# Kernel tuning notes

Measured on AMD Instinct MI355X. Metric: run time of the kernel, lower is better.

Reference implementation:

```python
import jax, jax.numpy as jnp
import numpy as np

K_NEIGHBORS = 10
SINKHORN_REG = 0.1
SINKHORN_ITERS = 50
EPS = 1e-10


def _pairwise_dist(x):
    # Euclidean cdist; clamp avoids sqrt(0) NaN grads on the diagonal
    sq = jnp.sum(x * x, axis=1)
    d2 = sq[:, None] + sq[None, :] - 2.0 * (x @ x.T)
    return jnp.sqrt(jnp.maximum(d2, 1e-12))


def setup_inputs() -> dict:
    key = jax.random.key(0)
    k1, k2 = jax.random.split(key)
    n, d = 8192, 128
    return {
        "embeddings": jax.random.normal(k1, (n, d), dtype=jnp.float32),
        "reference_embeddings": jax.random.normal(k2, (n, d), dtype=jnp.float32),
    }


def reference(embeddings, reference_embeddings):
    k = min(K_NEIGHBORS, embeddings.shape[0] - 1)

    cur_d = _pairwise_dist(embeddings)              # [n, n]
    ref_d = _pairwise_dist(reference_embeddings)    # [n, n]

    # k+1 smallest (ascending), drop self-distance column
    cur_knn = jnp.sort(cur_d, axis=1)[:, 1:k + 1]   # [n, k]
    ref_knn = jnp.sort(ref_d, axis=1)[:, 1:k + 1]   # [n, k]

    a = cur_knn / (jnp.sum(cur_knn, axis=1, keepdims=True) + EPS)  # [n, k]
    b = ref_knn / (jnp.sum(ref_knn, axis=1, keepdims=True) + EPS)  # [n, k]

    idx = jnp.arange(k, dtype=jnp.float32)
    M = jnp.abs(idx[None, :] - idx[:, None]) / k    # [k, k] shared cost
    Kmat = jnp.exp(-M / SINKHORN_REG)               # [k, k]

    # Batched Sinkhorn across all n samples at once
    def step(u, _):
        v = b / (u @ Kmat + EPS)          # K.T @ u per sample (K symmetric; explicit form u @ K)
        u = a / (v @ Kmat.T + EPS)        # K @ v per sample
        return u, None

    u0 = jnp.ones_like(a)
    u, _ = jax.lax.scan(step, u0, None, length=SINKHORN_ITERS)
    v = b / (u @ Kmat + EPS)

    # sum_ij u_i K_ij M_ij v_j per sample, then mean over n
    per_sample = jnp.einsum('ni,ij,nj->n', u, Kmat * M, v)
    return jnp.mean(per_sample)
```

## Files before the change

kernel.cpp:

```cpp
#include <hip/hip_runtime.h>
#include <hip/hip_bf16.h>
#include <math.h>

#define N 8192
#define D 128
#define NELEM (N * D)
#define KNN 10
#define EPSF 1e-10f
#define RT 64
#define NSLICE 8
#define RH 1024
#define BIGF 3.0e38f

typedef unsigned short ushort_t;
typedef short bf16x8 __attribute__((ext_vector_type(8)));
typedef float f32x4 __attribute__((ext_vector_type(4)));

template <int L>
__device__ __forceinline__ void insM(float (&l)[L], float v) {
  #pragma unroll
  for (int q = L - 1; q >= 1; --q)
    l[q] = __builtin_amdgcn_fmed3f(l[q - 1], l[q], v);
  l[0] = fminf(l[0], v);
}

__global__ void prep_kernel(const float* __restrict__ xc,
                            const float* __restrict__ xr,
                            ushort_t* __restrict__ xb,
                            ushort_t* __restrict__ xa,
                            float* __restrict__ sq) {
  int wid  = (blockIdx.x * blockDim.x + threadIdx.x) >> 6;
  int lane = threadIdx.x & 63;
  if (wid >= 2 * N) return;
  const float* x = (wid < N) ? xc : xr;
  int row = (wid < N) ? wid : wid - N;
  float2 v = *reinterpret_cast<const float2*>(x + (size_t)row * D + lane * 2);
  float s = v.x * v.x + v.y * v.y;
  #pragma unroll
  for (int off = 32; off; off >>= 1) s += __shfl_xor(s, off, 64);
  if (lane == 0) sq[wid] = s;
  auto cvt = [](float f) -> unsigned int {
    unsigned int b = __float_as_uint(f);
    return (b + 0x7FFFu + ((b >> 16) & 1u)) >> 16;
  };
  unsigned int pb = cvt(v.x) | (cvt(v.y) << 16);
  unsigned int pa = cvt(-2.f * v.x) | (cvt(-2.f * v.y) << 16);
  *reinterpret_cast<unsigned int*>(xb + (size_t)wid * D + lane * 2) = pb;
  *reinterpret_cast<unsigned int*>(xa + (size_t)wid * D + lane * 2) = pa;
}

__global__ __launch_bounds__(256, 4) void knn_mfma(
    const ushort_t* __restrict__ xb,
    const ushort_t* __restrict__ xa,
    const float* __restrict__ sq,
    float* __restrict__ partial) {
  __shared__ __align__(16) ushort_t Albuf[2][RT * D];
  __shared__ float sqbuf[2][RT];

  const int bid = blockIdx.x;
  const int mat = bid >> 9;
  const int colblk = (bid >> 3) & 63;
  const int slice = bid & 7;
  const ushort_t* __restrict__ XB = xb + (size_t)mat * NELEM;
  const ushort_t* __restrict__ XA = xa + (size_t)mat * NELEM;
  const float* __restrict__ SQ = sq + mat * N;
  const int r0 = slice * RH;
  const int t = threadIdx.x;
  const int w = t >> 6, l = t & 63;
  const int c0w = colblk * 128 + w * 32;

  bf16x8 bfr[2][4];
  #pragma unroll
  for (int j = 0; j < 2; ++j) {
    const ushort_t* p = XB + (size_t)(c0w + j * 16 + (l & 15)) * D + (l >> 4) * 8;
    #pragma unroll
    for (int kk = 0; kk < 4; ++kk)
      bfr[j][kk] = *reinterpret_cast<const bf16x8*>(p + kk * 32);
  }

  float cand[2][KNN];
  #pragma unroll
  for (int j = 0; j < 2; ++j)
    #pragma unroll
    for (int q = 0; q < KNN; ++q) cand[j][q] = BIGF;

  auto stage = [&](int tt, int bb) {
    const ushort_t* rowg = XA + (size_t)(r0 + tt * RT) * D;
    #pragma unroll
    for (int k2 = 0; k2 < 4; ++k2) {
      int s = w * 256 + k2 * 64 + l;
      int row = s >> 4, chslot = s & 15;
      int ch = (chslot & 8) | ((chslot & 7) ^ (row & 7));
      const ushort_t* g = rowg + row * D + ch * 8;
      ushort_t* dst = &Albuf[bb][(w * 256 + k2 * 64) * 8];
      __builtin_amdgcn_global_load_lds(
          (const __attribute__((address_space(1))) void*)g,
          (__attribute__((address_space(3))) void*)dst, 16, 0, 0);
    }
    if (w == 0) {
      const float* gs = SQ + r0 + tt * RT + l;
      float* dsts = &sqbuf[bb][0];
      __builtin_amdgcn_global_load_lds(
          (const __attribute__((address_space(1))) void*)gs,
          (__attribute__((address_space(3))) void*)dsts, 4, 0, 0);
    }
  };

  stage(0, 0);
  asm volatile("s_waitcnt vmcnt(0)" ::: "memory");
  __syncthreads();

  for (int tt = 0; tt < RH / RT; ++tt) {
    const int cur = tt & 1;
    if (tt < RH / RT - 1) stage(tt + 1, cur ^ 1);

    f32x4 sqi[4];
    #pragma unroll
    for (int i = 0; i < 4; ++i)
      sqi[i] = *reinterpret_cast<const f32x4*>(&sqbuf[cur][i * 16 + (l >> 4) * 4]);

    f32x4 acc[4][2];
    #pragma unroll
    for (int i = 0; i < 4; ++i)
      #pragma unroll
      for (int j = 0; j < 2; ++j) acc[i][j] = sqi[i];

    #pragma unroll
    for (int kk = 0; kk < 4; ++kk) {
      const int ch = kk * 4 + (l >> 4);
      const int chs = (ch & 8) | ((ch & 7) ^ (l & 7));
      bf16x8 af[4];
      #pragma unroll
      for (int i = 0; i < 4; ++i) {
        const int row = i * 16 + (l & 15);
        af[i] = *reinterpret_cast<const bf16x8*>(&Albuf[cur][(row * 16 + chs) * 8]);
      }
      #pragma unroll
      for (int i = 0; i < 4; ++i)
        #pragma unroll
        for (int j = 0; j < 2; ++j)
          acc[i][j] = __builtin_amdgcn_mfma_f32_16x16x32_bf16(af[i], bfr[j][kk],
                                                              acc[i][j], 0, 0, 0);
    }

    const int rbase = r0 + tt * RT;
    const unsigned diff = (unsigned)(c0w - rbase);
    if (diff < 64u) {
      #pragma unroll
      for (int i = 0; i < 4; ++i)
        #pragma unroll
        for (int j = 0; j < 2; ++j) {
          const int rr = (int)diff + j * 16 + (l & 15) - i * 16 - ((l >> 4) << 2);
          #pragma unroll
          for (int r = 0; r < 4; ++r)
            if (rr == r) acc[i][j][r] = BIGF;
        }
    }

    #pragma unroll
    for (int r = 0; r < 4; ++r)
      #pragma unroll
      for (int i = 0; i < 4; ++i)
        #pragma unroll
        for (int j = 0; j < 2; ++j)
          insM<KNN>(cand[j], acc[i][j][r]);

    asm volatile("s_waitcnt vmcnt(0)" ::: "memory");
    __syncthreads();
  }

  #pragma unroll
  for (int step = 16; step <= 32; step <<= 1)
    #pragma unroll
    for (int j = 0; j < 2; ++j)
      #pragma unroll
      for (int q = 0; q < KNN; ++q) {
        float o = __shfl_xor(cand[j][q], step, 64);
        insM<KNN>(cand[j], o);
      }

  if (l < 16) {
    #pragma unroll
    for (int j = 0; j < 2; ++j) {
      const int c = c0w + j * 16 + l;
      float* dst = partial + ((size_t)(mat * N + c) * NSLICE + slice) * KNN;
      #pragma unroll
      for (int q = 0; q < KNN; ++q) dst[q] = cand[j][q];
    }
  }
}

__global__ void merge_kernel(const float* __restrict__ partial,
                             const float* __restrict__ sq,
                             float* __restrict__ knn) {
  int idx = blockIdx.x * blockDim.x + threadIdx.x;
  if (idx >= 2 * N) return;
  float best[KNN];
  #pragma unroll
  for (int q = 0; q < KNN; ++q) best[q] = BIGF;
  const float* p = partial + (size_t)idx * NSLICE * KNN;
  for (int s = 0; s < NSLICE * KNN; ++s) insM<KNN>(best, p[s]);
  const float sqc = sq[idx];
  #pragma unroll
  for (int q = 0; q < KNN; ++q) {
    float d2 = best[q] + sqc;
    knn[(size_t)idx * KNN + q] = sqrtf(fmaxf(d2, 1e-12f));
  }
}

__global__ void sinkhorn_kernel(const float* __restrict__ knnc,
                                const float* __restrict__ knnr,
                                float* __restrict__ ps) {
  int s = blockIdx.x * blockDim.x + threadIdx.x;
  if (s >= N) return;
  constexpr float E1 = 0.36787944117144233f;
  float a[KNN], b[KNN];
  float suma = 0.f, sumb = 0.f;
  #pragma unroll
  for (int q = 0; q < KNN; ++q) { a[q] = knnc[(size_t)s * KNN + q]; suma += a[q]; }
  #pragma unroll
  for (int q = 0; q < KNN; ++q) { b[q] = knnr[(size_t)s * KNN + q]; sumb += b[q]; }
  float rsa = __builtin_amdgcn_rcpf(suma + EPSF);
  float rsb = __builtin_amdgcn_rcpf(sumb + EPSF);
  #pragma unroll
  for (int q = 0; q < KNN; ++q) { a[q] *= rsa; b[q] *= rsb; }

  float u_[KNN], v_[KNN];
  #pragma unroll
  for (int q = 0; q < KNN; ++q) u_[q] = 1.f;

  #pragma unroll 1
  for (int it = 0; it < 50; ++it) {
    float L[KNN], S[KNN];
    L[0] = u_[0];
    #pragma unroll
    for (int q = 1; q < KNN; ++q) L[q] = fmaf(E1, L[q - 1], u_[q]);
    S[KNN - 1] = u_[KNN - 1];
    #pragma unroll
    for (int q = KNN - 2; q >= 0; --q) S[q] = fmaf(E1, S[q + 1], u_[q]);
    #pragma unroll
    for (int q = 0; q < KNN; ++q) {
      float den = (q < KNN - 1) ? fmaf(E1, S[q + 1], L[q]) : L[KNN - 1];
      v_[q] = b[q] * __builtin_amdgcn_rcpf(den + EPSF);
    }
    L[0] = v_[0];
    #pragma unroll
    for (int q = 1; q < KNN; ++q) L[q] = fmaf(E1, L[q - 1], v_[q]);
    S[KNN - 1] = v_[KNN - 1];
    #pragma unroll
    for (int q = KNN - 2; q >= 0; --q) S[q] = fmaf(E1, S[q + 1], v_[q]);
    #pragma unroll
    for (int q = 0; q < KNN; ++q) {
      float den = (q < KNN - 1) ? fmaf(E1, S[q + 1], L[q]) : L[KNN - 1];
      u_[q] = a[q] * __builtin_amdgcn_rcpf(den + EPSF);
    }
  }
  {
    float L[KNN], S[KNN];
    L[0] = u_[0];
    #pragma unroll
    for (int q = 1; q < KNN; ++q) L[q] = fmaf(E1, L[q - 1], u_[q]);
    S[KNN - 1] = u_[KNN - 1];
    #pragma unroll
    for (int q = KNN - 2; q >= 0; --q) S[q] = fmaf(E1, S[q + 1], u_[q]);
    #pragma unroll
    for (int q = 0; q < KNN; ++q) {
      float den = (q < KNN - 1) ? fmaf(E1, S[q + 1], L[q]) : L[KNN - 1];
      v_[q] = b[q] * __builtin_amdgcn_rcpf(den + EPSF);
    }
  }
  float cost = 0.f;
  #pragma unroll
  for (int i = 0; i < KNN; ++i) {
    float accr = 0.f;
    #pragma unroll
    for (int j = 0; j < KNN; ++j) {
      const int dd = i > j ? i - j : j - i;
      const float wgt = 0.1f * (float)dd * __builtin_expf(-(float)dd);
      accr = fmaf(wgt, v_[j], accr);
    }
    cost = fmaf(u_[i], accr, cost);
  }
  ps[s] = cost;
}

__global__ void reduce_kernel(const float* __restrict__ ps, float* __restrict__ out) {
  __shared__ float red[256];
  int tid = threadIdx.x;
  float s = 0.f;
  for (int i = tid; i < N; i += 256) s += ps[i];
  red[tid] = s;
  __syncthreads();
  #pragma unroll
  for (int off = 128; off > 0; off >>= 1) {
    if (tid < off) red[tid] += red[tid + off];
    __syncthreads();
  }
  if (tid == 0) out[0] = red[0] * (1.0f / N);
}

extern "C" void kernel_launch(void* const* d_in, const int* in_sizes, int n_in,
                              void* d_out, int out_size, void* d_ws, size_t ws_size,
                              hipStream_t stream) {
  const float* xc = (const float*)d_in[0];
  const float* xr = (const float*)d_in[1];
  float* out = (float*)d_out;
  char* wsb = (char*)d_ws;

  float* sq       = (float*)wsb;
  ushort_t* xb    = (ushort_t*)(wsb + (1u << 16));
  ushort_t* xa    = (ushort_t*)(wsb + (1u << 16) + (4u << 20));
  float* partial  = (float*)(wsb + (1u << 16) + (8u << 20));
  float* knn      = partial + (size_t)2 * N * NSLICE * KNN;
  float* ps       = knn + (size_t)2 * N * KNN;

  prep_kernel<<<dim3(2 * N / 4), dim3(256), 0, stream>>>(xc, xr, xb, xa, sq);
  knn_mfma<<<dim3(1024), dim3(256), 0, stream>>>(xb, xa, sq, partial);
  merge_kernel<<<dim3((2 * N + 255) / 256), dim3(256), 0, stream>>>(partial, sq, knn);
  sinkhorn_kernel<<<dim3(N / 64), dim3(64), 0, stream>>>(knn, knn + (size_t)N * KNN, ps);
  reduce_kernel<<<dim3(1), dim3(256), 0, stream>>>(ps, out);
}
```

Measured before the change: 110.6 us.

## Shrink KNN row tile, preload squared norms once, fuse merge into Sinkhorn

Halves the row tile in the MFMA KNN kernel to 32 rows and stores A fragments in LDS in MFMA-native order, so they can be read contiguously without XOR swizzling. All 1024 squared norms of the slice are loaded into LDS once instead of per tile. The separate merge kernel is folded into the Sinkhorn kernel, which removes one launch and the intermediate knn buffer. The cost is twice as many loop iterations and barriers in the KNN kernel, and a serial merge that now runs inside the Sinkhorn kernel with only N threads instead of 2N.

```diff
diff --git a/kernel.cpp b/kernel.cpp
--- a/kernel.cpp
+++ b/kernel.cpp
@@ -7,7 +7,7 @@
 #define NELEM (N * D)
 #define KNN 10
 #define EPSF 1e-10f
-#define RT 64
+#define RT 32
 #define NSLICE 8
 #define RH 1024
 #define BIGF 3.0e38f
@@ -54,8 +54,8 @@
     const ushort_t* __restrict__ xa,
     const float* __restrict__ sq,
     float* __restrict__ partial) {
-  __shared__ __align__(16) ushort_t Albuf[2][RT * D];
-  __shared__ float sqbuf[2][RT];
+  __shared__ __align__(16) ushort_t Abuf[2][RT * D];
+  __shared__ __align__(16) float SQs[RH];
 
   const int bid = blockIdx.x;
   const int mat = bid >> 9;
@@ -69,6 +69,14 @@
   const int w = t >> 6, l = t & 63;
   const int c0w = colblk * 128 + w * 32;
 
+  {
+    const float* gs = SQ + r0 + w * 256 + l * 4;
+    float* dsts = &SQs[w * 256];
+    __builtin_amdgcn_global_load_lds(
+        (const __attribute__((address_space(1))) void*)gs,
+        (__attribute__((address_space(3))) void*)dsts, 16, 0, 0);
+  }
+
   bf16x8 bfr[2][4];
   #pragma unroll
   for (int j = 0; j < 2; ++j) {
@@ -87,23 +95,17 @@
   auto stage = [&](int tt, int bb) {
     const ushort_t* rowg = XA + (size_t)(r0 + tt * RT) * D;
     #pragma unroll
-    for (int k2 = 0; k2 < 4; ++k2) {
-      int s = w * 256 + k2 * 64 + l;
-      int row = s >> 4, chslot = s & 15;
-      int ch = (chslot & 8) | ((chslot & 7) ^ (row & 7));
+    for (int h = 0; h < 2; ++h) {
+      const int rg = 2 * w + h;
+      const int kk = rg >> 1, ii = rg & 1;
+      const int row = ii * 16 + (l & 15);
+      const int ch  = kk * 4 + (l >> 4);
       const ushort_t* g = rowg + row * D + ch * 8;
-      ushort_t* dst = &Albuf[bb][(w * 256 + k2 * 64) * 8];
+      ushort_t* dst = &Abuf[bb][rg * 512];
       __builtin_amdgcn_global_load_lds(
           (const __attribute__((address_space(1))) void*)g,
           (__attribute__((address_space(3))) void*)dst, 16, 0, 0);
     }
-    if (w == 0) {
-      const float* gs = SQ + r0 + tt * RT + l;
-      float* dsts = &sqbuf[bb][0];
-      __builtin_amdgcn_global_load_lds(
-          (const __attribute__((address_space(1))) void*)gs,
-          (__attribute__((address_space(3))) void*)dsts, 4, 0, 0);
-    }
   };
 
   stage(0, 0);
@@ -114,29 +116,27 @@
     const int cur = tt & 1;
     if (tt < RH / RT - 1) stage(tt + 1, cur ^ 1);
 
-    f32x4 sqi[4];
-    #pragma unroll
-    for (int i = 0; i < 4; ++i)
-      sqi[i] = *reinterpret_cast<const f32x4*>(&sqbuf[cur][i * 16 + (l >> 4) * 4]);
-
-    f32x4 acc[4][2];
-    #pragma unroll
-    for (int i = 0; i < 4; ++i)
+    f32x4 sqi[2];
+    #pragma unroll
+    for (int i = 0; i < 2; ++i)
+      sqi[i] = *reinterpret_cast<const f32x4*>(
+          &SQs[tt * RT + i * 16 + ((l >> 4) << 2)]);
+
+    f32x4 acc[2][2];
+    #pragma unroll
+    for (int i = 0; i < 2; ++i)
       #pragma unroll
       for (int j = 0; j < 2; ++j) acc[i][j] = sqi[i];
 
     #pragma unroll
     for (int kk = 0; kk < 4; ++kk) {
-      const int ch = kk * 4 + (l >> 4);
-      const int chs = (ch & 8) | ((ch & 7) ^ (l & 7));
-      bf16x8 af[4];
-      #pragma unroll
-      for (int i = 0; i < 4; ++i) {
-        const int row = i * 16 + (l & 15);
-        af[i] = *reinterpret_cast<const bf16x8*>(&Albuf[cur][(row * 16 + chs) * 8]);
-      }
-      #pragma unroll
-      for (int i = 0; i < 4; ++i)
+      bf16x8 af[2];
+      #pragma unroll
+      for (int i = 0; i < 2; ++i)
+        af[i] = *reinterpret_cast<const bf16x8*>(
+            &Abuf[cur][(kk * 2 + i) * 512 + l * 8]);
+      #pragma unroll
+      for (int i = 0; i < 2; ++i)
         #pragma unroll
         for (int j = 0; j < 2; ++j)
           acc[i][j] = __builtin_amdgcn_mfma_f32_16x16x32_bf16(af[i], bfr[j][kk],
@@ -144,23 +144,23 @@
     }
 
     const int rbase = r0 + tt * RT;
-    const unsigned diff = (unsigned)(c0w - rbase);
-    if (diff < 64u) {
-      #pragma unroll
-      for (int i = 0; i < 4; ++i)
+    const int idiff = c0w - rbase;
+    if ((unsigned)(idiff + 31) < 63u) {
+      #pragma unroll
+      for (int i = 0; i < 2; ++i)
         #pragma unroll
         for (int j = 0; j < 2; ++j) {
-          const int rr = (int)diff + j * 16 + (l & 15) - i * 16 - ((l >> 4) << 2);
+          const int dd = idiff + j * 16 + (l & 15) - i * 16 - ((l >> 4) << 2);
           #pragma unroll
           for (int r = 0; r < 4; ++r)
-            if (rr == r) acc[i][j][r] = BIGF;
+            if (dd == r) acc[i][j][r] = BIGF;
         }
     }
 
     #pragma unroll
     for (int r = 0; r < 4; ++r)
       #pragma unroll
-      for (int i = 0; i < 4; ++i)
+      for (int i = 0; i < 2; ++i)
         #pragma unroll
         for (int j = 0; j < 2; ++j)
           insM<KNN>(cand[j], acc[i][j][r]);
@@ -190,36 +190,31 @@
   }
 }
 
-__global__ void merge_kernel(const float* __restrict__ partial,
-                             const float* __restrict__ sq,
-                             float* __restrict__ knn) {
-  int idx = blockIdx.x * blockDim.x + threadIdx.x;
-  if (idx >= 2 * N) return;
-  float best[KNN];
-  #pragma unroll
-  for (int q = 0; q < KNN; ++q) best[q] = BIGF;
-  const float* p = partial + (size_t)idx * NSLICE * KNN;
-  for (int s = 0; s < NSLICE * KNN; ++s) insM<KNN>(best, p[s]);
-  const float sqc = sq[idx];
-  #pragma unroll
-  for (int q = 0; q < KNN; ++q) {
-    float d2 = best[q] + sqc;
-    knn[(size_t)idx * KNN + q] = sqrtf(fmaxf(d2, 1e-12f));
-  }
-}
-
-__global__ void sinkhorn_kernel(const float* __restrict__ knnc,
-                                const float* __restrict__ knnr,
-                                float* __restrict__ ps) {
+__global__ void sink_kernel(const float* __restrict__ partial,
+                            const float* __restrict__ sq,
+                            float* __restrict__ ps) {
   int s = blockIdx.x * blockDim.x + threadIdx.x;
   if (s >= N) return;
   constexpr float E1 = 0.36787944117144233f;
+
   float a[KNN], b[KNN];
+  #pragma unroll
+  for (int m = 0; m < 2; ++m) {
+    float best[KNN];
+    #pragma unroll
+    for (int q = 0; q < KNN; ++q) best[q] = BIGF;
+    const float* p = partial + (size_t)(m * N + s) * NSLICE * KNN;
+    for (int c = 0; c < NSLICE * KNN; ++c) insM<KNN>(best, p[c]);
+    const float sqc = sq[m * N + s];
+    float* dst = m ? b : a;
+    #pragma unroll
+    for (int q = 0; q < KNN; ++q)
+      dst[q] = sqrtf(fmaxf(best[q] + sqc, 1e-12f));
+  }
+
   float suma = 0.f, sumb = 0.f;
   #pragma unroll
-  for (int q = 0; q < KNN; ++q) { a[q] = knnc[(size_t)s * KNN + q]; suma += a[q]; }
-  #pragma unroll
-  for (int q = 0; q < KNN; ++q) { b[q] = knnr[(size_t)s * KNN + q]; sumb += b[q]; }
+  for (int q = 0; q < KNN; ++q) { suma += a[q]; sumb += b[q]; }
   float rsa = __builtin_amdgcn_rcpf(suma + EPSF);
   float rsb = __builtin_amdgcn_rcpf(sumb + EPSF);
   #pragma unroll
@@ -311,12 +306,10 @@
   ushort_t* xb    = (ushort_t*)(wsb + (1u << 16));
   ushort_t* xa    = (ushort_t*)(wsb + (1u << 16) + (4u << 20));
   float* partial  = (float*)(wsb + (1u << 16) + (8u << 20));
-  float* knn      = partial + (size_t)2 * N * NSLICE * KNN;
-  float* ps       = knn + (size_t)2 * N * KNN;
+  float* ps       = partial + (size_t)2 * N * NSLICE * KNN;
 
   prep_kernel<<<dim3(2 * N / 4), dim3(256), 0, stream>>>(xc, xr, xb, xa, sq);
   knn_mfma<<<dim3(1024), dim3(256), 0, stream>>>(xb, xa, sq, partial);
-  merge_kernel<<<dim3((2 * N + 255) / 256), dim3(256), 0, stream>>>(partial, sq, knn);
-  sinkhorn_kernel<<<dim3(N / 64), dim3(64), 0, stream>>>(knn, knn + (size_t)N * KNN, ps);
+  sink_kernel<<<dim3(N / 64), dim3(64), 0, stream>>>(partial, sq, ps);
   reduce_kernel<<<dim3(1), dim3(256), 0, stream>>>(ps, out);
 }
```

After: 115.1 us. 1.04x slower.
